# Performance work log

Measured on AMD Instinct MI355X. Metric: run time of the kernel, lower is better.

## Reference

```python
import jax, jax.numpy as jnp
import numpy as np

B, T, W, R, N = 32, 256, 128, 4, 128
IFACE = R * W + 3 * W + 5 * R + 3   # 919
INSZ = (R + 1) * W                  # 640
DELTA = 1e-6

def _lstm_step(x, h, c, Wih, Whh, bih, bhh):
    g = x @ Wih.T + bih + h @ Whh.T + bhh
    i, f, gg, o = jnp.split(g, 4, axis=-1)
    c = jax.nn.sigmoid(f) * c + jax.nn.sigmoid(i) * jnp.tanh(gg)
    return jax.nn.sigmoid(o) * jnp.tanh(c), c

def _cosine(mem, keys):
    # mem [b,n,w], keys [b,h,w] -> [b,h,n]
    mn = mem / (jnp.linalg.norm(mem, axis=2, keepdims=True) + DELTA)
    kn = keys / (jnp.linalg.norm(keys, axis=2, keepdims=True) + DELTA)
    return jnp.einsum('bhw,bnw->bhn', kn, mn)

def _memory_step(xi, st):
    # xi: [b, IFACE] interface vector; st: DNC memory state
    mem, link, prec, rw, ww, usage = st
    b = xi.shape[0]
    o1 = R * W; o2 = o1 + R; o3 = o2 + W; o4 = o3 + 1
    o5 = o4 + W; o6 = o5 + W; o7 = o6 + R; o8 = o7 + 1; o9 = o8 + 1
    read_keys = jnp.tanh(xi[:, :o1].reshape(b, R, W))
    read_str = jax.nn.softplus(xi[:, o1:o2])
    write_key = jnp.tanh(xi[:, o2:o3])
    write_str = jax.nn.softplus(xi[:, o3:o4])
    erase = jax.nn.sigmoid(xi[:, o4:o5])
    write_vec = jnp.tanh(xi[:, o5:o6])
    free_gates = jax.nn.sigmoid(xi[:, o6:o7])
    alloc_gate = jax.nn.sigmoid(xi[:, o7:o8])
    write_gate = jax.nn.sigmoid(xi[:, o8:o9])
    read_modes = jax.nn.softmax(xi[:, o9:].reshape(b, R, 3), axis=-1)
    # usage vector update (single write head)
    usage = usage + (1 - usage) * ww
    usage = usage * jnp.prod(1 - free_gates[:, :, None] * rw, axis=1)
    # write content weighting [b,n]
    wc = jax.nn.softmax(_cosine(mem, write_key[:, None, :])[:, 0, :] * write_str, axis=1)
    # allocation weighting: sort ascending, exclusive cumprod, unsort
    u = DELTA + (1 - DELTA) * usage
    phi = jnp.argsort(u, axis=1)
    su = jnp.take_along_axis(u, phi, axis=1)
    prod_su = jnp.cumprod(jnp.concatenate([jnp.ones((b, 1), u.dtype), su], axis=1), axis=1)[:, :-1]
    alloc = jnp.take_along_axis((1 - su) * prod_su, jnp.argsort(phi, axis=1), axis=1)
    # write weighting [b,n]
    ww = write_gate * (alloc_gate * alloc + (1 - alloc_gate) * wc)
    # erase then write
    mem = mem * (1 - ww[:, :, None] * erase[:, None, :]) + ww[:, :, None] * write_vec[:, None, :]
    # temporal link matrix [b,n,n], zero diagonal
    link = (1 - ww[:, :, None] - ww[:, None, :]) * link + ww[:, :, None] * prec[:, None, :]
    link = link * (1 - jnp.eye(N, dtype=link.dtype))
    prec = (1 - jnp.sum(ww, axis=1, keepdims=True)) * prec + ww
    # read weighting: content + forward/backward temporal modes
    rc = jax.nn.softmax(_cosine(mem, read_keys) * read_str[:, :, None], axis=2)
    fw = jnp.einsum('bij,brj->bri', link, rw)
    bw = jnp.einsum('brj,bji->bri', rw, link)
    rw = read_modes[:, :, 0:1] * bw + read_modes[:, :, 1:2] * fw + read_modes[:, :, 2:3] * rc
    read_vecs = jnp.einsum('brn,bnw->bwr', rw, mem)  # [b,w,r] as used by controller
    return read_vecs, (mem, link, prec, rw, ww, usage)

def _forward(input, enc_Wih, enc_Whh, enc_bih, enc_bhh, ctl_Wih, ctl_Whh, ctl_bih, ctl_bhh, iface_W, iface_b, out_W, out_b):
    dt = input.dtype
    h0 = jnp.zeros((B, W), dt)
    def enc_step(carry, x_t):
        h, c = _lstm_step(x_t, carry[0], carry[1], enc_Wih, enc_Whh, enc_bih, enc_bhh)
        return (h, c), h
    _, enc = jax.lax.scan(enc_step, (h0, h0), jnp.swapaxes(input, 0, 1))  # enc: [T,B,W]
    z = lambda *s: jnp.zeros(s, dt)
    mem0 = (z(B, N, W), z(B, N, N), z(B, N), z(B, R, N), z(B, N), z(B, N))
    def step(carry, enc_t):
        h, c, rv, mst = carry
        # cat([b,w,1],[b,w,r]) then flatten -> interleaved per memory-cell element, as in torch
        x = jnp.concatenate([enc_t[:, :, None], rv], axis=2).reshape(B, INSZ)
        h, c = _lstm_step(x, h, c, ctl_Wih, ctl_Whh, ctl_bih, ctl_bhh)
        xi = h @ iface_W.T + iface_b
        rv, mst = _memory_step(xi, mst)
        out_t = jnp.concatenate([h, rv.reshape(B, W * R)], axis=1) @ out_W.T + out_b
        return (h, c, rv, mst), out_t
    _, outs = jax.lax.scan(step, (h0, h0, z(B, W, R), mem0), enc)
    return jnp.swapaxes(outs, 0, 1)  # [B,T,W]

def setup_inputs():
    key = jax.random.key(0)
    ks = jax.random.split(key, 8)
    p = lambda k, s: jax.random.normal(k, s, jnp.float32) * 0.05
    return {
        'input': jax.random.normal(ks[0], (B, T, W), jnp.float32),
        'source_lengths': jnp.full((B,), T, jnp.int32),
        'enc_Wih': p(ks[1], (4 * W, W)), 'enc_Whh': p(ks[2], (4 * W, W)),
        'enc_bih': jnp.zeros((4 * W,), jnp.float32), 'enc_bhh': jnp.zeros((4 * W,), jnp.float32),
        'ctl_Wih': p(ks[3], (4 * W, INSZ)), 'ctl_Whh': p(ks[4], (4 * W, W)),
        'ctl_bih': jnp.zeros((4 * W,), jnp.float32), 'ctl_bhh': jnp.zeros((4 * W,), jnp.float32),
        'iface_W': p(ks[5], (IFACE, W)), 'iface_b': jnp.zeros((IFACE,), jnp.float32),
        'out_W': p(ks[6], (W, INSZ)), 'out_b': jnp.zeros((W,), jnp.float32),
    }

def reference(input, source_lengths, enc_Wih, enc_Whh, enc_bih, enc_bhh, ctl_Wih, ctl_Whh, ctl_bih, ctl_bhh, iface_W, iface_b, out_W, out_b):
    # source_lengths are all == T (full-length sequences), so pack/pad is identity.
    return _forward(input, enc_Wih, enc_Whh, enc_bih, enc_bhh, ctl_Wih, ctl_Whh, ctl_bih, ctl_bhh, iface_W, iface_b, out_W, out_b)
```

## Files before the change

### kernel.cpp

```cpp
#include <hip/hip_runtime.h>

typedef unsigned short u16;
typedef unsigned int u32;

#define NT 1024
#define Bv 32
#define Tv 256
#define Wv 128
#define Rv 4
#define Nv 128
#define DELTAv 1e-6f

__device__ __forceinline__ float bf2f(u16 u){
  union { u32 i; float f; } c; c.i = ((u32)u) << 16; return c.f;
}
__device__ __forceinline__ u16 f2bf(float f){
  union { float f; u32 u; } c; c.f = f;
  u32 u = c.u;
  return (u16)((u + 0x7fffu + ((u >> 16) & 1u)) >> 16);
}
__device__ __forceinline__ void unp(u32 v, float& a, float& b){
  union { u32 i; float f; } c0, c1;
  c0.i = v << 16; c1.i = v & 0xffff0000u;
  a = c0.f; b = c1.f;
}
__device__ __forceinline__ float sigm(float x){ return 1.0f / (1.0f + __expf(-x)); }
__device__ __forceinline__ float softplusf(float x){ return fmaxf(x, 0.f) + log1pf(__expf(-fabsf(x))); }
__device__ __forceinline__ float wredsum(float v){
  #pragma unroll
  for (int o = 32; o > 0; o >>= 1) v += __shfl_down(v, o, 64);
  return v;
}
__device__ __forceinline__ float wredmax(float v){
  #pragma unroll
  for (int o = 32; o > 0; o >>= 1) v = fmaxf(v, __shfl_down(v, o, 64));
  return v;
}
__device__ __forceinline__ float ldval(const void* p, int idx, int dt32){
  return dt32 ? ((const float*)p)[idx] : bf2f(((const u16*)p)[idx]);
}
__device__ __forceinline__ float rl(float v, int l){
  union { int i; float f; } c;
  c.i = __builtin_amdgcn_readlane(__float_as_int(v), l);
  return c.f;
}

template<int ITERS, int STRIDE>
__device__ __forceinline__ float gemv_bf(const u32* __restrict__ wp, const float* __restrict__ xp){
  float a0 = 0.f, a1 = 0.f;
  u32 wb[8];
  #pragma unroll
  for (int i = 0; i < 8; i++) wb[i] = wp[i * STRIDE];
  #pragma unroll 1
  for (int c = 0; c < ITERS - 8; c += 8){
    u32 wn[8];
    #pragma unroll
    for (int i = 0; i < 8; i++) wn[i] = wp[(c + 8 + i) * STRIDE];
    #pragma unroll
    for (int i = 0; i < 8; i++){
      float w0, w1; unp(wb[i], w0, w1);
      float2 x2 = *(const float2*)(xp + 2 * (c + i));
      a0 = fmaf(x2.x, w0, a0); a1 = fmaf(x2.y, w1, a1);
      wb[i] = wn[i];
    }
  }
  #pragma unroll
  for (int i = 0; i < 8; i++){
    float w0, w1; unp(wb[i], w0, w1);
    float2 x2 = *(const float2*)(xp + 2 * (ITERS - 8 + i));
    a0 = fmaf(x2.x, w0, a0); a1 = fmaf(x2.y, w1, a1);
  }
  return a0 + a1;
}

template<int ITERS, int STRIDE>
__device__ __forceinline__ void gemv2_bf(const u32* __restrict__ wp0, const u32* __restrict__ wp1,
                                         const float* __restrict__ xp, float& r0, float& r1){
  float a0 = 0.f, a1 = 0.f, b0 = 0.f, b1 = 0.f;
  u32 wa[4], wb[4];
  #pragma unroll
  for (int i = 0; i < 4; i++){ wa[i] = wp0[i * STRIDE]; wb[i] = wp1[i * STRIDE]; }
  #pragma unroll 1
  for (int c = 0; c < ITERS - 4; c += 4){
    u32 na[4], nb[4];
    #pragma unroll
    for (int i = 0; i < 4; i++){ na[i] = wp0[(c + 4 + i) * STRIDE]; nb[i] = wp1[(c + 4 + i) * STRIDE]; }
    #pragma unroll
    for (int i = 0; i < 4; i++){
      float2 x2 = *(const float2*)(xp + 2 * (c + i));
      float w0, w1;
      unp(wa[i], w0, w1);
      a0 = fmaf(x2.x, w0, a0); a1 = fmaf(x2.y, w1, a1);
      unp(wb[i], w0, w1);
      b0 = fmaf(x2.x, w0, b0); b1 = fmaf(x2.y, w1, b1);
      wa[i] = na[i]; wb[i] = nb[i];
    }
  }
  #pragma unroll
  for (int i = 0; i < 4; i++){
    float2 x2 = *(const float2*)(xp + 2 * (ITERS - 4 + i));
    float w0, w1;
    unp(wa[i], w0, w1);
    a0 = fmaf(x2.x, w0, a0); a1 = fmaf(x2.y, w1, a1);
    unp(wb[i], w0, w1);
    b0 = fmaf(x2.x, w0, b0); b1 = fmaf(x2.y, w1, b1);
  }
  r0 = a0 + a1; r1 = b0 + b1;
}

__global__ void detect_dtype(const u16* __restrict__ buf, int* __restrict__ flag){
  int lane = threadIdx.x;
  float crazy = 0.f;
  for (int i = 0; i < 4; i++){
    u16 v = buf[lane * 4 + i];
    int e = (v >> 7) & 0xFF;
    if (e != 0 && (e < 117 || e > 137)) crazy += 1.f;
  }
  crazy = wredsum(crazy);
  if (lane == 0) flag[0] = (crazy >= 32.f) ? 1 : 0;
}

__device__ __forceinline__ u16 rdbf(const void* s, size_t idx, int f32){
  return f32 ? f2bf(((const float*)s)[idx]) : ((const u16*)s)[idx];
}

__global__ void pack_w(const void* __restrict__ src, u32* __restrict__ dst,
                       int Js, int Jd, int K, const int* __restrict__ flag){
  int j = blockIdx.x * 256 + threadIdx.x;
  int k2 = blockIdx.y;
  if (j >= Jd) return;
  u16 lo = 0, hi = 0;
  if (j < Js){
    lo = rdbf(src, (size_t)j * K + 2 * k2, flag[0]);
    hi = rdbf(src, (size_t)j * K + 2 * k2 + 1, flag[0]);
  }
  dst[(size_t)k2 * Jd + j] = (u32)lo | ((u32)hi << 16);
}

__device__ __forceinline__ int permctl(int c){
  if (c < 128) return 5 * c;
  int q = c - 128; return 5 * (q & 127) + 1 + (q >> 7);
}
__device__ __forceinline__ int permout(int c){
  if (c < 128) return c;
  int q = c - 128; return 128 + 4 * (q & 127) + (q >> 7);
}

__global__ void pack_ctl(const void* __restrict__ src, u32* __restrict__ dst,
                         const int* __restrict__ flag){
  int j = blockIdx.x * 256 + threadIdx.x;
  int k2 = blockIdx.y;
  if (j >= 512) return;
  u16 lo = rdbf(src, (size_t)j * 640 + permctl(2 * k2), flag[0]);
  u16 hi = rdbf(src, (size_t)j * 640 + permctl(2 * k2 + 1), flag[0]);
  dst[(size_t)k2 * 512 + j] = (u32)lo | ((u32)hi << 16);
}

__global__ void pack_out(const void* __restrict__ src, u32* __restrict__ dst,
                         const int* __restrict__ flag){
  int j = threadIdx.x;
  int k2 = blockIdx.y;
  if (j >= 128) return;
  u16 lo = rdbf(src, (size_t)j * 640 + permout(2 * k2), flag[0]);
  u16 hi = rdbf(src, (size_t)j * 640 + permout(2 * k2 + 1), flag[0]);
  dst[(size_t)k2 * 128 + j] = (u32)lo | ((u32)hi << 16);
}

__global__ void fill_half(u16* __restrict__ p, int n){
  int i = blockIdx.x * 256 + threadIdx.x;
  if (i < n) p[i] = 0x3F00;
}

__global__ __launch_bounds__(NT) void dnc_main(
    const void* __restrict__ input,
    const void* __restrict__ enc_bih_g, const void* __restrict__ enc_bhh_g,
    const void* __restrict__ ctl_bih_g, const void* __restrict__ ctl_bhh_g,
    const void* __restrict__ iface_b_g, const void* __restrict__ out_b_g,
    const u32* __restrict__ encPW, const u32* __restrict__ ctlPW,
    const u32* __restrict__ ifPW, const u32* __restrict__ outPW,
    void* __restrict__ outp, const int* __restrict__ dtflag)
{
  const int bid = blockIdx.x;
  const int tid = threadIdx.x;
  const int lane = tid & 63;
  const int wid = tid >> 6;
  const int dt32 = dtflag[0];

  __shared__ __align__(16) float memS[Nv * 129];
  __shared__ __align__(16) float linkS[Nv * 129];
  __shared__ __align__(16) float pp[NT];
  __shared__ __align__(16) float ppE[NT];
  __shared__ __align__(16) float xhC[768];
  __shared__ __align__(16) float xin2[2][128];
  __shared__ __align__(16) float rkeyS[512], rwS[512], rcS[512];
  __shared__ __align__(16) float wkeyS[128], eraseS[128], wvecS[128];
  __shared__ __align__(16) float wwS[128], usageS[128], precS[128], wcS[128];
  __shared__ __align__(16) float uS[128], sortedU[128], scanA[128], alS[128], sqS[128];
  __shared__ __align__(16) float encBias[512], ctlBias[512];
  __shared__ __align__(16) float outBias[128];
  __shared__ float rstrS[4], fgS[4], rmRaw[12], rmS[12], scal[16];

  float cE = 0.f;
  float cC = 0.f;

  if (tid < 512){
    encBias[tid] = ldval(enc_bih_g, tid, dt32) + ldval(enc_bhh_g, tid, dt32);
    ctlBias[tid] = ldval(ctl_bih_g, tid, dt32) + ldval(ctl_bhh_g, tid, dt32);
    rwS[tid] = 0.f;
  }
  if (tid < 768) xhC[tid] = 0.f;
  if (tid < 128){
    outBias[tid] = ldval(out_b_g, tid, dt32);
    wwS[tid] = 0.f; usageS[tid] = 0.f; precS[tid] = 0.f;
  }
  for (int i = tid; i < Nv * 129; i += NT){ memS[i] = 0.f; linkS[i] = 0.f; }
  if (tid < 64){
    int idx = (bid * Tv + 0) * Wv + 2 * tid;
    xin2[0][2 * tid] = ldval(input, idx, dt32);
    xin2[0][2 * tid + 1] = ldval(input, idx + 1, dt32);
  } else if (tid >= 64 && tid < 128){
    int w2 = (tid - 64) * 2;
    int idx = (bid * Tv + 1) * Wv + w2;
    xin2[1][w2] = ldval(input, idx, dt32);
    xin2[1][w2 + 1] = ldval(input, idx + 1, dt32);
  }
  __syncthreads();

  if (tid >= 512 && tid < 768){
    int o = tid - 512;
    float r0, r1;
    gemv2_bf<64, 512>(encPW + o, encPW + o + 256, xin2[0], r0, r1);
    rcS[o] = r0; rcS[o + 256] = r1;
  }
  __syncthreads();
  if (tid >= 896){
    int w = tid - 896;
    float g0 = rcS[w] + encBias[w];
    float g1 = rcS[128 + w] + encBias[128 + w];
    float g2 = rcS[256 + w] + encBias[256 + w];
    float g3 = rcS[384 + w] + encBias[384 + w];
    float cn = sigm(g1) * cE + sigm(g0) * tanhf(g2);
    cE = cn;
    xhC[w] = sigm(g3) * tanhf(cn);
  }
  __syncthreads();

  for (int t = 0; t < Tv; ++t){
    if (tid < 512){
      int s = tid >> 8, o = tid & 255;
      float r0, r1;
      gemv2_bf<192, 512>(ctlPW + (s * 192) * 512 + o, ctlPW + (s * 192) * 512 + o + 256,
                         xhC + s * 384, r0, r1);
      pp[s * 512 + o] = r0;
      pp[s * 512 + o + 256] = r1;
    } else if (tid < 768){
      int o = tid - 512;
      float r0, r1;
      gemv2_bf<64, 512>(encPW + o, encPW + o + 256, xin2[(t + 1) & 1], r0, r1);
      rcS[o] = r0; rcS[o + 256] = r1;
    } else {
      int q = tid - 768;
      int s = q >> 7, j = q & 127;
      ppE[q] = gemv_bf<128, 128>(outPW + (64 + s * 128) * 128 + j, xhC + 128 + 256 * s);
    }
    __syncthreads();

    if (tid < 128){
      float g0 = pp[tid] + pp[512 + tid] + ctlBias[tid];
      float g1 = pp[128 + tid] + pp[640 + tid] + ctlBias[128 + tid];
      float g2 = pp[256 + tid] + pp[768 + tid] + ctlBias[256 + tid];
      float g3 = pp[384 + tid] + pp[896 + tid] + ctlBias[384 + tid];
      float cn = sigm(g1) * cC + sigm(g0) * tanhf(g2);
      cC = cn;
      xhC[640 + tid] = sigm(g3) * tanhf(cn);
    } else if (tid < 256){
      if (t > 0){
        int w = tid - 128;
        float o = outBias[w] + ppE[w] + ppE[128 + w]
                + ppE[512 + w] + ppE[640 + w] + ppE[768 + w] + ppE[896 + w];
        size_t oi = ((size_t)bid * Tv + (t - 1)) * Wv + w;
        if (dt32) ((float*)outp)[oi] = o;
        else ((u16*)outp)[oi] = f2bf(o);
      }
    } else if (tid >= 512 && tid < 768){
      int o = tid - 512;
      float r0, r1;
      gemv2_bf<64, 512>(encPW + 64 * 512 + o, encPW + 64 * 512 + o + 256, xhC, r0, r1);
      rcS[o] = rcS[o] + r0;
      rcS[o + 256] = rcS[o + 256] + r1;
    } else if (tid >= 768 && tid < 832){
      int w2 = (tid - 768) * 2;
      int col = (t + 2 < Tv) ? t + 2 : Tv - 1;
      int idx = (bid * Tv + col) * Wv + w2;
      xin2[t & 1][w2] = ldval(input, idx, dt32);
      xin2[t & 1][w2 + 1] = ldval(input, idx + 1, dt32);
    }
    __syncthreads();

    if (tid < 464){
      float r0, r1;
      gemv2_bf<64, 928>(ifPW + tid, ifPW + tid + 464, xhC + 640, r0, r1);
      pp[tid] = r0 + ldval(iface_b_g, tid, dt32);
      pp[tid + 464] = r1 + ((tid + 464 < 919) ? ldval(iface_b_g, tid + 464, dt32) : 0.f);
    } else if (tid >= 896){
      int w = tid - 896;
      float g0 = rcS[w] + encBias[w];
      float g1 = rcS[128 + w] + encBias[128 + w];
      float g2 = rcS[256 + w] + encBias[256 + w];
      float g3 = rcS[384 + w] + encBias[384 + w];
      float cn = sigm(g1) * cE + sigm(g0) * tanhf(g2);
      cE = cn;
      xhC[w] = sigm(g3) * tanhf(cn);
    }
    __syncthreads();

    if (tid < 919){
      float v = pp[tid];
      if (tid < 512) rkeyS[tid] = tanhf(v);
      else if (tid < 516) rstrS[tid - 512] = softplusf(v);
      else if (tid < 644) wkeyS[tid - 516] = tanhf(v);
      else if (tid == 644) scal[0] = softplusf(v);
      else if (tid < 773) eraseS[tid - 645] = sigm(v);
      else if (tid < 901) wvecS[tid - 773] = tanhf(v);
      else if (tid < 905) fgS[tid - 901] = sigm(v);
      else if (tid == 905) scal[1] = sigm(v);
      else if (tid == 906) scal[2] = sigm(v);
      else rmRaw[tid - 907] = v;
    }
    __syncthreads();

    if (tid < 256){
      int n = tid & 127, hf = tid >> 7;
      float wk = wkeyS[hf * 64 + lane];
      const float* mrow = memS + n * 129 + hf * 64;
      float dt = 0.f;
      #pragma unroll 64
      for (int jj = 0; jj < 64; jj++) dt = fmaf(rl(wk, jj), mrow[jj], dt);
      pp[tid] = dt;
    } else if (tid < 512){
      int r = wid - 4;
      float a = rkeyS[r * 128 + lane], b = rkeyS[r * 128 + 64 + lane];
      float s = wredsum(a * a + b * b);
      if (lane == 0) scal[4 + r] = 1.f / (sqrtf(s) + DELTAv);
    } else if (tid < 576){
      float a = wkeyS[lane], b = wkeyS[64 + lane];
      float s = wredsum(a * a + b * b);
      if (lane == 0) scal[8] = 1.f / (sqrtf(s) + DELTAv);
    } else if (tid < 704){
      int n = tid - 576;
      float us = usageS[n];
      us = us + (1.f - us) * wwS[n];
      float ret = (1.f - fgS[0] * rwS[n]) * (1.f - fgS[1] * rwS[128 + n]) *
                  (1.f - fgS[2] * rwS[256 + n]) * (1.f - fgS[3] * rwS[384 + n]);
      us *= ret;
      usageS[n] = us;
      uS[n] = DELTAv + (1.f - DELTAv) * us;
    } else if (tid < 960){
      int q = tid - 704;
      int n = q & 127, hf = q >> 7;
      const float* mrow = memS + n * 129 + hf * 64;
      float sq = 0.f;
      #pragma unroll 64
      for (int jj = 0; jj < 64; jj++){ float m = mrow[jj]; sq = fmaf(m, m, sq); }
      pp[tid] = sq;
    } else if (tid < 964){
      int r = tid - 960;
      float m0 = rmRaw[3 * r], m1 = rmRaw[3 * r + 1], m2 = rmRaw[3 * r + 2];
      float mx = fmaxf(m0, fmaxf(m1, m2));
      float e0 = __expf(m0 - mx), e1 = __expf(m1 - mx), e2 = __expf(m2 - mx);
      float s = e0 + e1 + e2;
      rmS[3 * r] = e0 / s; rmS[3 * r + 1] = e1 / s; rmS[3 * r + 2] = e2 / s;
    }
    __syncthreads();

    if (wid == 0){
      float d0 = pp[lane] + pp[128 + lane];
      float d1 = pp[64 + lane] + pp[192 + lane];
      float q0 = pp[704 + lane] + pp[832 + lane];
      float q1 = pp[768 + lane] + pp[896 + lane];
      float kfac = scal[8] * scal[0];
      float a  = d0 / (sqrtf(q0) + DELTAv) * kfac;
      float bq = d1 / (sqrtf(q1) + DELTAv) * kfac;
      float mx = wredmax(fmaxf(a, bq)); mx = __shfl(mx, 0, 64);
      float ea = __expf(a - mx), eb = __expf(bq - mx);
      float s = wredsum(ea + eb); s = __shfl(s, 0, 64);
      wcS[lane] = ea / s; wcS[lane + 64] = eb / s;
    } else if (wid == 1){
      int l = lane;
      float u0 = uS[l], u1 = uS[64 + l];
      int r0 = 0, r1 = 0;
      for (int m = 0; m < 128; m++){
        float um = uS[m];
        r0 += (um < u0) || (um == u0 && m < l);
        r1 += (um < u1) || (um == u1 && m < 64 + l);
      }
      sortedU[r0] = u0; sortedU[r1] = u1;
      float a = sortedU[2 * l], bq = sortedU[2 * l + 1];
      float p = a * bq;
      float incl = p;
      #pragma unroll
      for (int o = 1; o < 64; o <<= 1){
        float tv = __shfl_up(incl, o, 64);
        if (l >= o) incl *= tv;
      }
      float exh = __shfl_up(incl, 1, 64);
      if (l == 0) exh = 1.f;
      scanA[2 * l] = exh;
      scanA[2 * l + 1] = exh * a;
      float ex0 = scanA[r0], ex1 = scanA[r1];
      alS[l] = (1.f - u0) * ex0;
      alS[64 + l] = (1.f - u1) * ex1;
    }
    __syncthreads();

    if (wid == 0){
      float w0v = scal[2] * (scal[1] * alS[lane] + (1.f - scal[1]) * wcS[lane]);
      float w1v = scal[2] * (scal[1] * alS[64 + lane] + (1.f - scal[1]) * wcS[64 + lane]);
      wwS[lane] = w0v; wwS[64 + lane] = w1v;
      float s = wredsum(w0v + w1v);
      if (lane == 0) scal[3] = s;
    }
    __syncthreads();

    #pragma unroll
    for (int it = 0; it < 16; it++){
      int e = it * NT + tid;
      int n = e >> 7, w = e & 127;
      float wwn = wwS[n];
      float m = memS[n * 129 + w];
      memS[n * 129 + w] = m * (1.f - wwn * eraseS[w]) + wwn * wvecS[w];
      float l = linkS[n * 129 + w];
      linkS[n * 129 + w] = (n == w) ? 0.f
        : ((1.f - wwn - wwS[w]) * l + wwn * precS[w]);
    }
    __syncthreads();

    if (tid < 256){
      int i = tid & 127, rg = tid >> 7;
      int rA = 2 * rg, rB = rA + 1;
      float rwA0 = rwS[rA * 128 + lane], rwA1 = rwS[rA * 128 + 64 + lane];
      float rwB0 = rwS[rB * 128 + lane], rwB1 = rwS[rB * 128 + 64 + lane];
      float fA = 0.f, fB = 0.f, bA = 0.f, bB = 0.f;
      #pragma unroll 128
      for (int j = 0; j < 128; j++){
        float lr = linkS[i * 129 + j];
        float lc = linkS[j * 129 + i];
        float wA = rl((j < 64) ? rwA0 : rwA1, j & 63);
        float wB = rl((j < 64) ? rwB0 : rwB1, j & 63);
        fA = fmaf(wA, lr, fA); bA = fmaf(wA, lc, bA);
        fB = fmaf(wB, lr, fB); bB = fmaf(wB, lc, bB);
      }
      pp[rA * 128 + i] = fA; pp[rB * 128 + i] = fB;
      pp[512 + rA * 128 + i] = bA; pp[512 + rB * 128 + i] = bB;
    } else if (tid < 512){
      int q = tid - 256;
      int n = q & 127, rg = q >> 7;
      int rA = 2 * rg, rB = rA + 1;
      float kA0 = rkeyS[rA * 128 + lane], kA1 = rkeyS[rA * 128 + 64 + lane];
      float kB0 = rkeyS[rB * 128 + lane], kB1 = rkeyS[rB * 128 + 64 + lane];
      float sq = 0.f, dA = 0.f, dB = 0.f;
      #pragma unroll 128
      for (int j = 0; j < 128; j++){
        float m = memS[n * 129 + j];
        if (rg == 0) sq = fmaf(m, m, sq);
        dA = fmaf(rl((j < 64) ? kA0 : kA1, j & 63), m, dA);
        dB = fmaf(rl((j < 64) ? kB0 : kB1, j & 63), m, dB);
      }
      rcS[rA * 128 + n] = dA;
      rcS[rB * 128 + n] = dB;
      if (rg == 0) sqS[n] = sq;
    } else {
      int s = (tid - 512) >> 7, j = tid & 127;
      ppE[tid] = gemv_bf<16, 128>(outPW + (s * 16) * 128 + j, xhC + 640 + 32 * s);
    }
    __syncthreads();

    if (wid < 4){
      int r = wid;
      float fac = scal[4 + r] * rstrS[r];
      float im0 = 1.f / (sqrtf(sqS[lane]) + DELTAv);
      float im1 = 1.f / (sqrtf(sqS[64 + lane]) + DELTAv);
      float a  = rcS[r * 128 + lane] * im0 * fac;
      float bq = rcS[r * 128 + 64 + lane] * im1 * fac;
      float mx = wredmax(fmaxf(a, bq)); mx = __shfl(mx, 0, 64);
      float ea = __expf(a - mx), eb = __expf(bq - mx);
      float s = wredsum(ea + eb); s = __shfl(s, 0, 64);
      float pa = ea / s, pb = eb / s;
      int o0 = r * 128 + lane, o1 = o0 + 64;
      rwS[o0] = rmS[3 * r] * pp[512 + o0] + rmS[3 * r + 1] * pp[o0] + rmS[3 * r + 2] * pa;
      rwS[o1] = rmS[3 * r] * pp[512 + o1] + rmS[3 * r + 1] * pp[o1] + rmS[3 * r + 2] * pb;
    } else if (tid >= 256 && tid < 384){
      int n = tid - 256;
      precS[n] = (1.f - scal[3]) * precS[n] + wwS[n];
    }
    __syncthreads();

    if (tid < 512){
      int r = tid >> 7, w = tid & 127;
      float rw0 = rwS[r * 128 + lane], rw1 = rwS[r * 128 + 64 + lane];
      float acc = 0.f;
      #pragma unroll 128
      for (int n = 0; n < 128; n++)
        acc = fmaf(rl((n < 64) ? rw0 : rw1, n & 63), memS[n * 129 + w], acc);
      xhC[128 + tid] = acc;
    }
    __syncthreads();
  }

  if (tid < 256){
    int s = tid >> 7, j = tid & 127;
    ppE[tid] = gemv_bf<128, 128>(outPW + (64 + s * 128) * 128 + j, xhC + 128 + 256 * s);
  }
  __syncthreads();
  if (tid < 128){
    float o = outBias[tid] + ppE[tid] + ppE[128 + tid]
            + ppE[512 + tid] + ppE[640 + tid] + ppE[768 + tid] + ppE[896 + tid];
    size_t oi = ((size_t)bid * Tv + (Tv - 1)) * Wv + tid;
    if (dt32) ((float*)outp)[oi] = o;
    else ((u16*)outp)[oi] = f2bf(o);
  }
}

extern "C" void kernel_launch(void* const* d_in, const int* in_sizes, int n_in,
                              void* d_out, int out_size, void* d_ws, size_t ws_size,
                              hipStream_t stream) {
  (void)in_sizes; (void)n_in;
  const void* input   = d_in[0];
  const void* enc_Wih = d_in[2];
  const void* enc_Whh = d_in[3];
  const void* enc_bih = d_in[4];
  const void* enc_bhh = d_in[5];
  const void* ctl_Wih = d_in[6];
  const void* ctl_Whh = d_in[7];
  const void* ctl_bih = d_in[8];
  const void* ctl_bhh = d_in[9];
  const void* iface_W = d_in[10];
  const void* iface_b = d_in[11];
  const void* out_W   = d_in[12];
  const void* out_b   = d_in[13];

  char* ws = (char*)d_ws;
  size_t off = 0;
  int* dtflag = (int*)(ws + off); off += 256;
  u32* encPW = (u32*)(ws + off); off += (size_t)128 * 512 * 4;
  u32* ctlPW = (u32*)(ws + off); off += (size_t)384 * 512 * 4;
  u32* ifPW  = (u32*)(ws + off); off += (size_t)64 * 928 * 4;
  u32* outPW = (u32*)(ws + off); off += (size_t)320 * 128 * 4;
  const size_t need_bytes = off;

  if (ws_size < need_bytes){
    fill_half<<<dim3((out_size + 255) / 256), dim3(256), 0, stream>>>((u16*)d_out, out_size);
    return;
  }

  detect_dtype<<<dim3(1), dim3(64), 0, stream>>>((const u16*)input, dtflag);

  pack_w<<<dim3(2, 64), 256, 0, stream>>>(enc_Wih, encPW, 512, 512, 128, dtflag);
  pack_w<<<dim3(2, 64), 256, 0, stream>>>(enc_Whh, encPW + 64 * 512, 512, 512, 128, dtflag);
  pack_ctl<<<dim3(2, 320), 256, 0, stream>>>(ctl_Wih, ctlPW, dtflag);
  pack_w<<<dim3(2, 64), 256, 0, stream>>>(ctl_Whh, ctlPW + 320 * 512, 512, 512, 128, dtflag);
  pack_w<<<dim3(4, 64), 256, 0, stream>>>(iface_W, ifPW, 919, 928, 128, dtflag);
  pack_out<<<dim3(1, 320), 128, 0, stream>>>(out_W, outPW, dtflag);

  dnc_main<<<dim3(Bv), dim3(NT), 0, stream>>>(
      input, enc_bih, enc_bhh, ctl_bih, ctl_bhh, iface_b, out_b,
      encPW, ctlPW, ifPW, outPW, d_out, dtflag);
}
```

Measured before the change: 9.014 ms.

## Fuse interface activation into gemv, merge usage/sort and write-weight phases, rebalance link/read work

Applies the interface nonlinearities directly in the iface gemv threads, removing one block-wide barrier and a shared round trip. The usage update moves into the allocation-sort wave and the content softmax into the write-weight wave, removing another barrier per step. The link/read-content phase is split so each thread handles one read head, spreading it over all 1024 threads, and the output gemv moves to a later phase. The cost is longer serial chains in a few single-wave phases, which could lengthen the critical path.

Measured after the change: 9.470 ms. 5.1% more time.

```diff
diff --git a/kernel.cpp b/kernel.cpp
--- a/kernel.cpp
+++ b/kernel.cpp
@@ -194,7 +194,7 @@
   __shared__ __align__(16) float xin2[2][128];
   __shared__ __align__(16) float rkeyS[512], rwS[512], rcS[512];
   __shared__ __align__(16) float wkeyS[128], eraseS[128], wvecS[128];
-  __shared__ __align__(16) float wwS[128], usageS[128], precS[128], wcS[128];
+  __shared__ __align__(16) float wwS[128], usageS[128], precS[128];
   __shared__ __align__(16) float uS[128], sortedU[128], scanA[128], alS[128], sqS[128];
   __shared__ __align__(16) float encBias[512], ctlBias[512];
   __shared__ __align__(16) float outBias[128];
@@ -202,6 +202,19 @@
 
   float cE = 0.f;
   float cC = 0.f;
+
+  auto scatter_xi = [&](int c, float v){
+    if (c < 512) rkeyS[c] = tanhf(v);
+    else if (c < 516) rstrS[c - 512] = softplusf(v);
+    else if (c < 644) wkeyS[c - 516] = tanhf(v);
+    else if (c == 644) scal[0] = softplusf(v);
+    else if (c < 773) eraseS[c - 645] = sigm(v);
+    else if (c < 901) wvecS[c - 773] = tanhf(v);
+    else if (c < 905) fgS[c - 901] = sigm(v);
+    else if (c == 905) scal[1] = sigm(v);
+    else if (c == 906) scal[2] = sigm(v);
+    else rmRaw[c - 907] = v;
+  };
 
   if (tid < 512){
     encBias[tid] = ldval(enc_bih_g, tid, dt32) + ldval(enc_bhh_g, tid, dt32);
@@ -300,8 +313,9 @@
     if (tid < 464){
       float r0, r1;
       gemv2_bf<64, 928>(ifPW + tid, ifPW + tid + 464, xhC + 640, r0, r1);
-      pp[tid] = r0 + ldval(iface_b_g, tid, dt32);
-      pp[tid + 464] = r1 + ((tid + 464 < 919) ? ldval(iface_b_g, tid + 464, dt32) : 0.f);
+      scatter_xi(tid, r0 + ldval(iface_b_g, tid, dt32));
+      int c1 = tid + 464;
+      if (c1 < 919) scatter_xi(c1, r1 + ldval(iface_b_g, c1, dt32));
     } else if (tid >= 896){
       int w = tid - 896;
       float g0 = rcS[w] + encBias[w];
@@ -311,21 +325,6 @@
       float cn = sigm(g1) * cE + sigm(g0) * tanhf(g2);
       cE = cn;
       xhC[w] = sigm(g3) * tanhf(cn);
-    }
-    __syncthreads();
-
-    if (tid < 919){
-      float v = pp[tid];
-      if (tid < 512) rkeyS[tid] = tanhf(v);
-      else if (tid < 516) rstrS[tid - 512] = softplusf(v);
-      else if (tid < 644) wkeyS[tid - 516] = tanhf(v);
-      else if (tid == 644) scal[0] = softplusf(v);
-      else if (tid < 773) eraseS[tid - 645] = sigm(v);
-      else if (tid < 901) wvecS[tid - 773] = tanhf(v);
-      else if (tid < 905) fgS[tid - 901] = sigm(v);
-      else if (tid == 905) scal[1] = sigm(v);
-      else if (tid == 906) scal[2] = sigm(v);
-      else rmRaw[tid - 907] = v;
     }
     __syncthreads();
 
@@ -346,48 +345,28 @@
       float a = wkeyS[lane], b = wkeyS[64 + lane];
       float s = wredsum(a * a + b * b);
       if (lane == 0) scal[8] = 1.f / (sqrtf(s) + DELTAv);
-    } else if (tid < 704){
-      int n = tid - 576;
-      float us = usageS[n];
-      us = us + (1.f - us) * wwS[n];
-      float ret = (1.f - fgS[0] * rwS[n]) * (1.f - fgS[1] * rwS[128 + n]) *
-                  (1.f - fgS[2] * rwS[256 + n]) * (1.f - fgS[3] * rwS[384 + n]);
-      us *= ret;
-      usageS[n] = us;
-      uS[n] = DELTAv + (1.f - DELTAv) * us;
-    } else if (tid < 960){
-      int q = tid - 704;
+    } else if (tid < 832){
+      int q = tid - 576;
       int n = q & 127, hf = q >> 7;
       const float* mrow = memS + n * 129 + hf * 64;
       float sq = 0.f;
       #pragma unroll 64
       for (int jj = 0; jj < 64; jj++){ float m = mrow[jj]; sq = fmaf(m, m, sq); }
-      pp[tid] = sq;
-    } else if (tid < 964){
-      int r = tid - 960;
-      float m0 = rmRaw[3 * r], m1 = rmRaw[3 * r + 1], m2 = rmRaw[3 * r + 2];
-      float mx = fmaxf(m0, fmaxf(m1, m2));
-      float e0 = __expf(m0 - mx), e1 = __expf(m1 - mx), e2 = __expf(m2 - mx);
-      float s = e0 + e1 + e2;
-      rmS[3 * r] = e0 / s; rmS[3 * r + 1] = e1 / s; rmS[3 * r + 2] = e2 / s;
-    }
-    __syncthreads();
-
-    if (wid == 0){
-      float d0 = pp[lane] + pp[128 + lane];
-      float d1 = pp[64 + lane] + pp[192 + lane];
-      float q0 = pp[704 + lane] + pp[832 + lane];
-      float q1 = pp[768 + lane] + pp[896 + lane];
-      float kfac = scal[8] * scal[0];
-      float a  = d0 / (sqrtf(q0) + DELTAv) * kfac;
-      float bq = d1 / (sqrtf(q1) + DELTAv) * kfac;
-      float mx = wredmax(fmaxf(a, bq)); mx = __shfl(mx, 0, 64);
-      float ea = __expf(a - mx), eb = __expf(bq - mx);
-      float s = wredsum(ea + eb); s = __shfl(s, 0, 64);
-      wcS[lane] = ea / s; wcS[lane + 64] = eb / s;
-    } else if (wid == 1){
+      pp[512 + q] = sq;
+    } else if (tid < 896){
       int l = lane;
-      float u0 = uS[l], u1 = uS[64 + l];
+      float us0 = usageS[l], us1 = usageS[64 + l];
+      us0 = us0 + (1.f - us0) * wwS[l];
+      us1 = us1 + (1.f - us1) * wwS[64 + l];
+      float ret0 = (1.f - fgS[0] * rwS[l]) * (1.f - fgS[1] * rwS[128 + l]) *
+                   (1.f - fgS[2] * rwS[256 + l]) * (1.f - fgS[3] * rwS[384 + l]);
+      float ret1 = (1.f - fgS[0] * rwS[64 + l]) * (1.f - fgS[1] * rwS[192 + l]) *
+                   (1.f - fgS[2] * rwS[320 + l]) * (1.f - fgS[3] * rwS[448 + l]);
+      us0 *= ret0; us1 *= ret1;
+      usageS[l] = us0; usageS[64 + l] = us1;
+      float u0 = DELTAv + (1.f - DELTAv) * us0;
+      float u1 = DELTAv + (1.f - DELTAv) * us1;
+      uS[l] = u0; uS[64 + l] = u1;
       int r0 = 0, r1 = 0;
       for (int m = 0; m < 128; m++){
         float um = uS[m];
@@ -410,15 +389,33 @@
       float ex0 = scanA[r0], ex1 = scanA[r1];
       alS[l] = (1.f - u0) * ex0;
       alS[64 + l] = (1.f - u1) * ex1;
+    } else if (tid < 900){
+      int r = tid - 896;
+      float m0 = rmRaw[3 * r], m1 = rmRaw[3 * r + 1], m2 = rmRaw[3 * r + 2];
+      float mx = fmaxf(m0, fmaxf(m1, m2));
+      float e0 = __expf(m0 - mx), e1 = __expf(m1 - mx), e2 = __expf(m2 - mx);
+      float s = e0 + e1 + e2;
+      rmS[3 * r] = e0 / s; rmS[3 * r + 1] = e1 / s; rmS[3 * r + 2] = e2 / s;
     }
     __syncthreads();
 
     if (wid == 0){
-      float w0v = scal[2] * (scal[1] * alS[lane] + (1.f - scal[1]) * wcS[lane]);
-      float w1v = scal[2] * (scal[1] * alS[64 + lane] + (1.f - scal[1]) * wcS[64 + lane]);
+      float d0 = pp[lane] + pp[128 + lane];
+      float d1 = pp[64 + lane] + pp[192 + lane];
+      float q0 = pp[512 + lane] + pp[640 + lane];
+      float q1 = pp[576 + lane] + pp[704 + lane];
+      float kfac = scal[8] * scal[0];
+      float a  = d0 / (sqrtf(q0) + DELTAv) * kfac;
+      float bq = d1 / (sqrtf(q1) + DELTAv) * kfac;
+      float mx = wredmax(fmaxf(a, bq)); mx = __shfl(mx, 0, 64);
+      float ea = __expf(a - mx), eb = __expf(bq - mx);
+      float s = wredsum(ea + eb); s = __shfl(s, 0, 64);
+      float wc0 = ea / s, wc1 = eb / s;
+      float w0v = scal[2] * (scal[1] * alS[lane] + (1.f - scal[1]) * wc0);
+      float w1v = scal[2] * (scal[1] * alS[64 + lane] + (1.f - scal[1]) * wc1);
       wwS[lane] = w0v; wwS[64 + lane] = w1v;
-      float s = wredsum(w0v + w1v);
-      if (lane == 0) scal[3] = s;
+      float s2 = wredsum(w0v + w1v);
+      if (lane == 0) scal[3] = s2;
     }
     __syncthreads();
 
@@ -435,43 +432,32 @@
     }
     __syncthreads();
 
-    if (tid < 256){
-      int i = tid & 127, rg = tid >> 7;
-      int rA = 2 * rg, rB = rA + 1;
-      float rwA0 = rwS[rA * 128 + lane], rwA1 = rwS[rA * 128 + 64 + lane];
-      float rwB0 = rwS[rB * 128 + lane], rwB1 = rwS[rB * 128 + 64 + lane];
-      float fA = 0.f, fB = 0.f, bA = 0.f, bB = 0.f;
+    if (tid < 512){
+      int r = wid >> 1, i = tid & 127;
+      float rw0 = rwS[r * 128 + lane], rw1 = rwS[r * 128 + 64 + lane];
+      float f = 0.f, b = 0.f;
       #pragma unroll 128
       for (int j = 0; j < 128; j++){
         float lr = linkS[i * 129 + j];
         float lc = linkS[j * 129 + i];
-        float wA = rl((j < 64) ? rwA0 : rwA1, j & 63);
-        float wB = rl((j < 64) ? rwB0 : rwB1, j & 63);
-        fA = fmaf(wA, lr, fA); bA = fmaf(wA, lc, bA);
-        fB = fmaf(wB, lr, fB); bB = fmaf(wB, lc, bB);
+        float w = rl((j < 64) ? rw0 : rw1, j & 63);
+        f = fmaf(w, lr, f); b = fmaf(w, lc, b);
       }
-      pp[rA * 128 + i] = fA; pp[rB * 128 + i] = fB;
-      pp[512 + rA * 128 + i] = bA; pp[512 + rB * 128 + i] = bB;
-    } else if (tid < 512){
-      int q = tid - 256;
-      int n = q & 127, rg = q >> 7;
-      int rA = 2 * rg, rB = rA + 1;
-      float kA0 = rkeyS[rA * 128 + lane], kA1 = rkeyS[rA * 128 + 64 + lane];
-      float kB0 = rkeyS[rB * 128 + lane], kB1 = rkeyS[rB * 128 + 64 + lane];
-      float sq = 0.f, dA = 0.f, dB = 0.f;
+      pp[r * 128 + i] = f;
+      pp[512 + r * 128 + i] = b;
+    } else {
+      int q = tid - 512;
+      int r = q >> 7, n = q & 127;
+      float k0 = rkeyS[r * 128 + lane], k1 = rkeyS[r * 128 + 64 + lane];
+      float sq = 0.f, d = 0.f;
       #pragma unroll 128
       for (int j = 0; j < 128; j++){
         float m = memS[n * 129 + j];
-        if (rg == 0) sq = fmaf(m, m, sq);
-        dA = fmaf(rl((j < 64) ? kA0 : kA1, j & 63), m, dA);
-        dB = fmaf(rl((j < 64) ? kB0 : kB1, j & 63), m, dB);
+        if (r == 0) sq = fmaf(m, m, sq);
+        d = fmaf(rl((j < 64) ? k0 : k1, j & 63), m, d);
       }
-      rcS[rA * 128 + n] = dA;
-      rcS[rB * 128 + n] = dB;
-      if (rg == 0) sqS[n] = sq;
-    } else {
-      int s = (tid - 512) >> 7, j = tid & 127;
-      ppE[tid] = gemv_bf<16, 128>(outPW + (s * 16) * 128 + j, xhC + 640 + 32 * s);
+      rcS[r * 128 + n] = d;
+      if (r == 0) sqS[n] = sq;
     }
     __syncthreads();
 
@@ -492,6 +478,9 @@
     } else if (tid >= 256 && tid < 384){
       int n = tid - 256;
       precS[n] = (1.f - scal[3]) * precS[n] + wwS[n];
+    } else if (tid >= 512){
+      int s = (tid - 512) >> 7, j = tid & 127;
+      ppE[tid] = gemv_bf<16, 128>(outPW + (s * 16) * 128 + j, xhC + 640 + 32 * s);
     }
     __syncthreads();
 
```
